# Performance work log

Measured on AMD Instinct MI355X. Metric: run time of the kernel, lower is better.

Reference implementation:

```python
import jax, jax.numpy as jnp
import numpy as np

N = 50000      # nodes
E = 800000     # edges (before self-loops)
H = 2          # attention heads
C = 64         # hidden_channels (per-head out since concat=False)
L = 3          # num_layers - 2 conv blocks
OUT = 128      # readout out_channels
G = 512        # num graphs
VOCAB = 100    # embedding table size
NEG_SLOPE = 0.2


def setup_inputs() -> dict:
    key = jax.random.key(0)
    ks = jax.random.split(key, 12)
    s = 1.0 / np.sqrt(C)
    x = jax.random.randint(ks[0], (N,), 0, VOCAB, dtype=jnp.int32)
    edge_index = jax.random.randint(ks[1], (2, E), 0, N, dtype=jnp.int32)
    batch = jnp.sort(jax.random.randint(ks[2], (N,), 0, G, dtype=jnp.int32))
    embed = jax.random.normal(ks[3], (VOCAB, C), dtype=jnp.float32) * s
    lin_W = jax.random.normal(ks[4], (L, C, C), dtype=jnp.float32) * s
    lin_b = jnp.zeros((L, C), dtype=jnp.float32)
    gat_Wl = jax.random.normal(ks[5], (L, C, H * C), dtype=jnp.float32) * s
    gat_bl = jnp.zeros((L, H * C), dtype=jnp.float32)
    gat_Wr = jax.random.normal(ks[6], (L, C, H * C), dtype=jnp.float32) * s
    gat_br = jnp.zeros((L, H * C), dtype=jnp.float32)
    gat_att = jax.random.normal(ks[7], (L, H, C), dtype=jnp.float32) * s
    gat_bias = jnp.zeros((L, C), dtype=jnp.float32)
    readout_W = jax.random.normal(ks[8], (C, OUT), dtype=jnp.float32) * s
    readout_b = jnp.zeros((OUT,), dtype=jnp.float32)
    return {"x": x, "edge_index": edge_index, "batch": batch, "num_graphs": G,
            "embed": embed, "lin_W": lin_W, "lin_b": lin_b,
            "gat_Wl": gat_Wl, "gat_bl": gat_bl, "gat_Wr": gat_Wr, "gat_br": gat_br,
            "gat_att": gat_att, "gat_bias": gat_bias,
            "readout_W": readout_W, "readout_b": readout_b}


def _gatv2_layer(h, src, dst, Wl, bl, Wr, br, att, bias):
    # lin_l -> source/message features, lin_r -> target features (PyG GATv2Conv)
    xl = (h @ Wl + bl).reshape(N, H, C)
    xr = (h @ Wr + br).reshape(N, H, C)
    # per-edge GATv2 score: a^T LeakyReLU(x_l[j] + x_r[i])
    e = jax.nn.leaky_relu(xl[src] + xr[dst], NEG_SLOPE)      # [E2,H,C]
    score = jnp.einsum('ehc,hc->eh', e, att)                 # [E2,H]
    # segment softmax over incoming edges of each dst node (stable)
    m = jax.lax.stop_gradient(jax.ops.segment_max(score, dst, num_segments=N))
    p = jnp.exp(score - m[dst])
    denom = jax.ops.segment_sum(p, dst, num_segments=N)      # [N,H]
    alpha = p / denom[dst]                                   # [E2,H]
    msg = xl[src] * alpha[:, :, None]                        # [E2,H,C]
    agg = jax.ops.segment_sum(msg, dst, num_segments=N)      # [N,H,C]
    return agg.mean(axis=1) + bias                           # concat=False -> head mean


def reference(x, edge_index, batch, num_graphs, embed, lin_W, lin_b,
              gat_Wl, gat_bl, gat_Wr, gat_br, gat_att, gat_bias,
              readout_W, readout_b):
    # add self loops (GATv2Conv default add_self_loops=True)
    loops = jnp.arange(N, dtype=edge_index.dtype)
    src = jnp.concatenate([edge_index[0], loops])
    dst = jnp.concatenate([edge_index[1], loops])
    h = embed[x]                                             # [N,C]
    for l in range(L):
        h = jax.nn.relu(h @ lin_W[l] + lin_b[l])             # dropout is a no-op in eval
        h = _gatv2_layer(h, src, dst, gat_Wl[l], gat_bl[l], gat_Wr[l], gat_br[l],
                         gat_att[l], gat_bias[l])
    out = h @ readout_W + readout_b                          # [N,OUT]
    return jax.ops.segment_sum(out, batch, num_segments=num_graphs)  # [G,OUT]
```

## Files before the change

### kernel.cpp

```cpp
#include <hip/hip_runtime.h>
#include <hip/hip_fp16.h>

#define N_NODES  50000
#define E_EDGES  800000
#define E_TOT    850000
#define H_HEADS  2
#define C_DIM    64
#define HC       128
#define L_LAYERS 3
#define OUT_DIM  128
#define G_GRAPHS 512
#define NEG_SLOPE 0.2f
#define NB       196
#define EPB      4096

typedef float v2f __attribute__((ext_vector_type(2)));

__device__ __forceinline__ void lds_fence() { asm volatile("" ::: "memory"); }

__global__ void init_kernel(float* __restrict__ out, int* __restrict__ bucket_counts) {
    int i = blockIdx.x * 256 + threadIdx.x;
    if (i < G_GRAPHS * OUT_DIM) out[i] = 0.f;
    if (blockIdx.x == 0) bucket_counts[threadIdx.x] = 0;
}

__global__ void bucket_count_kernel(const int* __restrict__ dsts, int* __restrict__ bucket_counts) {
    __shared__ int hist[256];
    int tid = threadIdx.x;
    hist[tid] = 0;
    __syncthreads();
    int ebase = blockIdx.x * EPB;
#pragma unroll
    for (int i = 0; i < 16; i++) {
        int e = ebase + i * 256 + tid;
        if (e < E_TOT) {
            int d = (e < E_EDGES) ? dsts[e] : e - E_EDGES;
            atomicAdd(&hist[d >> 8], 1);
        }
    }
    __syncthreads();
    if (hist[tid]) atomicAdd(&bucket_counts[tid], hist[tid]);
}

__global__ void scan196_kernel(const int* __restrict__ bucket_counts,
                               int* __restrict__ bwptr, int* __restrict__ bbase) {
    __shared__ int wsum[4];
    int tid = threadIdx.x;
    int lane = tid & 63, wid = tid >> 6;
    int cnt = (tid < NB) ? bucket_counts[tid] : 0;
    int v = cnt;
#pragma unroll
    for (int off = 1; off < 64; off <<= 1) {
        int t = __shfl_up(v, off, 64);
        if (lane >= off) v += t;
    }
    if (lane == 63) wsum[wid] = v;
    __syncthreads();
    int woff = 0;
#pragma unroll
    for (int w = 0; w < 4; w++) if (w < wid) woff += wsum[w];
    v += woff;
    if (tid < NB) { bwptr[tid] = v - cnt; bbase[tid] = v - cnt; }
    if (tid == 0) bbase[NB] = E_TOT;
}

__global__ void edge_partition_kernel(const int* __restrict__ srcs, const int* __restrict__ dsts,
                                      int* __restrict__ bwptr, unsigned int* __restrict__ ebuf) {
    __shared__ int hist[256];
    __shared__ int lscan[256];
    __shared__ int sExcl[256];
    __shared__ int lcnt[256];
    __shared__ int gbase[256];
    __shared__ unsigned int sval[EPB];
    __shared__ unsigned char sgid[EPB];
    int tid = threadIdx.x;
    int ebase = blockIdx.x * EPB;
    hist[tid] = 0;
    __syncthreads();
    unsigned int val[16];
    int gid[16];
#pragma unroll
    for (int i = 0; i < 16; i++) {
        int e = ebase + i * 256 + tid;
        if (e < E_TOT) {
            int s, d;
            if (e < E_EDGES) { s = srcs[e]; d = dsts[e]; }
            else             { s = d = e - E_EDGES; }
            val[i] = ((unsigned)s << 8) | (unsigned)(d & 255);
            gid[i] = d >> 8;
            atomicAdd(&hist[gid[i]], 1);
        } else gid[i] = -1;
    }
    __syncthreads();
    lscan[tid] = hist[tid];
    __syncthreads();
#pragma unroll
    for (int off = 1; off < 256; off <<= 1) {
        int t = (tid >= off) ? lscan[tid - off] : 0;
        __syncthreads();
        lscan[tid] += t;
        __syncthreads();
    }
    sExcl[tid] = lscan[tid] - hist[tid];
    lcnt[tid] = 0;
    __syncthreads();
#pragma unroll
    for (int i = 0; i < 16; i++) {
        if (gid[i] >= 0) {
            int off = atomicAdd(&lcnt[gid[i]], 1);
            int idx = sExcl[gid[i]] + off;
            sval[idx] = val[i];
            sgid[idx] = (unsigned char)gid[i];
        }
    }
    if (tid < NB) {
        int c = hist[tid];
        gbase[tid] = c ? atomicAdd(&bwptr[tid], c) : 0;
    }
    __syncthreads();
    int total = lscan[255];
    for (int idx = tid; idx < total; idx += 256) {
        int g = sgid[idx];
        ebuf[gbase[g] + (idx - sExcl[g])] = sval[idx];
    }
}

__global__ void bucket_csr_kernel(const unsigned int* __restrict__ ebuf,
                                  const int* __restrict__ bbase,
                                  int* __restrict__ row_ptr,
                                  unsigned short* __restrict__ src_sorted) {
    __shared__ int hist[256];
    __shared__ int lcnt[256];
    __shared__ int wsum[4];
    int g = blockIdx.x, tid = threadIdx.x;
    int n0 = g << 8;
    int nodes = min(256, N_NODES - n0);
    int b0 = bbase[g], b1 = bbase[g + 1];
    int cnt = b1 - b0;
    hist[tid] = 0;
    lcnt[tid] = 0;
    __syncthreads();
    for (int i = tid; i < cnt; i += 256) atomicAdd(&hist[ebuf[b0 + i] & 255], 1);
    __syncthreads();
    int c = hist[tid];
    int v = c;
    int lane = tid & 63, wid = tid >> 6;
#pragma unroll
    for (int off = 1; off < 64; off <<= 1) {
        int t = __shfl_up(v, off, 64);
        if (lane >= off) v += t;
    }
    if (lane == 63) wsum[wid] = v;
    __syncthreads();
    int woff = 0;
#pragma unroll
    for (int w = 0; w < 4; w++) if (w < wid) woff += wsum[w];
    v += woff;
    int nbase = b0 + v - c;
    if (tid < nodes) row_ptr[n0 + tid] = nbase;
    if (g == NB - 1 && tid == 0) row_ptr[N_NODES] = E_TOT;
    __syncthreads();
    hist[tid] = nbase;
    __syncthreads();
    for (int i = tid; i < cnt; i += 256) {
        unsigned int e = ebuf[b0 + i];
        int dl = e & 255;
        int slot = hist[dl] + atomicAdd(&lcnt[dl], 1);
        src_sorted[slot] = (unsigned short)(e >> 8);
    }
}

__global__ void layer_lin_kernel(const float* __restrict__ h,
                                 const int* __restrict__ xs, const float* __restrict__ etab,
                                 int use_embed,
                                 const float* __restrict__ W, const float* __restrict__ b,
                                 const float* __restrict__ Wl, const float* __restrict__ bl,
                                 const float* __restrict__ Wr, const float* __restrict__ br,
                                 __half* __restrict__ xlh, float* __restrict__ xri) {
    __shared__ float sH[16 * 64];
    __shared__ float sH2[16 * 64];
    int tid = threadIdx.x;
    int base = blockIdx.x * 16;
#pragma unroll
    for (int i = 0; i < 4; i++) {
        int idx = tid + i * 256;
        int nn = base + (idx >> 6);
        int cc = idx & 63;
        float hv = 0.f;
        if (nn < N_NODES)
            hv = use_embed ? etab[xs[nn] * 64 + cc] : h[(size_t)nn * 64 + cc];
        sH[idx] = hv;
    }
    __syncthreads();
    {
        int c = tid & 63, g = tid >> 6;
        float a0 = b[c], a1 = a0, a2 = a0, a3 = a0;
        for (int k = 0; k < 64; k++) {
            float wv = W[k * 64 + c];
            a0 = fmaf(sH[(g * 4 + 0) * 64 + k], wv, a0);
            a1 = fmaf(sH[(g * 4 + 1) * 64 + k], wv, a1);
            a2 = fmaf(sH[(g * 4 + 2) * 64 + k], wv, a2);
            a3 = fmaf(sH[(g * 4 + 3) * 64 + k], wv, a3);
        }
        sH2[(g * 4 + 0) * 64 + c] = fmaxf(a0, 0.f);
        sH2[(g * 4 + 1) * 64 + c] = fmaxf(a1, 0.f);
        sH2[(g * 4 + 2) * 64 + c] = fmaxf(a2, 0.f);
        sH2[(g * 4 + 3) * 64 + c] = fmaxf(a3, 0.f);
    }
    __syncthreads();
    {
        int j = tid & 127, gg = tid >> 7;
        float accl[8], accr[8];
#pragma unroll
        for (int n = 0; n < 8; n++) { accl[n] = bl[j]; accr[n] = br[j]; }
        for (int k = 0; k < 64; k++) {
            float wl = Wl[k * 128 + j], wr = Wr[k * 128 + j];
#pragma unroll
            for (int n = 0; n < 8; n++) {
                float hv = sH2[(gg * 8 + n) * 64 + k];
                accl[n] = fmaf(hv, wl, accl[n]);
                accr[n] = fmaf(hv, wr, accr[n]);
            }
        }
        int hh = j >> 6, c = j & 63;
#pragma unroll
        for (int n = 0; n < 8; n++) {
            int node = base + gg * 8 + n;
            if (node < N_NODES) {
                size_t o = (size_t)node * 128 + c * 2 + hh;
                xlh[o] = __float2half(accl[n]);
                xri[o] = accr[n];
            }
        }
    }
}

__global__ void gat_kernel(const __half2* __restrict__ xlh, const float2* __restrict__ xr2,
                           const float* __restrict__ att, const int* __restrict__ row_ptr,
                           const unsigned short* __restrict__ src_sorted,
                           const float* __restrict__ bias,
                           float* __restrict__ h_out) {
    __shared__ __align__(16) float cbuf[4][8 * 132];
    int w = threadIdx.x >> 6;
    int d = blockIdx.x * 4 + w;
    if (d >= N_NODES) return;
    int lane = threadIdx.x & 63;
    int r0 = row_ptr[d], r1 = row_ptr[d + 1];
    float2 vrf = xr2[(size_t)d * 64 + lane];
    v2f vr2 = {vrf.x, vrf.y};
    v2f att2 = {att[lane], att[64 + lane]};
    float* cb = cbuf[w];
    int e_of = lane >> 3, p = lane & 7;

    float dpx = 0.f, dpy = 0.f;
    v2f ac0 = {0.f, 0.f}, ac1 = {0.f, 0.f};

#define GAT_LOAD(V, CB) do {                                                    \
        int lim_ = nchunk - 1;                                                  \
        _Pragma("unroll")                                                       \
        for (int e = 0; e < 8; e++) {                                           \
            int ee_ = (CB) + e;                                                 \
            int sv_ = __builtin_amdgcn_readlane(idx, (ee_ < nchunk) ? ee_ : lim_); \
            V[e] = xlh[(size_t)sv_ * 64 + lane];                                \
        }                                                                       \
    } while (0)

#define GAT_PROC(V, CB) do {                                                    \
        int rem_ = nchunk - (CB);                                               \
        v2f vf8[8];                                                             \
        _Pragma("unroll")                                                       \
        for (int e = 0; e < 8; e++) {                                           \
            float2 vf_ = __half22float2(V[e]);                                  \
            v2f vl2 = {vf_.x, vf_.y};                                           \
            vf8[e] = vl2;                                                       \
            v2f z = vl2 + vr2;                                                  \
            v2f t = __builtin_elementwise_max(z, z * NEG_SLOPE) * att2;         \
            *(v2f*)&cb[e * 132 + 2 * lane] = t;                                 \
        }                                                                       \
        lds_fence();                                                            \
        v2f s2 = {0.f, 0.f};                                                    \
        {                                                                       \
            const float4* row_ = (const float4*)&cb[e_of * 132 + p * 16];       \
            _Pragma("unroll")                                                   \
            for (int j = 0; j < 4; j++) {                                       \
                float4 f = row_[j];                                             \
                s2 += (v2f){f.x, f.y};                                          \
                s2 += (v2f){f.z, f.w};                                          \
            }                                                                   \
        }                                                                       \
        lds_fence();                                                            \
        _Pragma("unroll")                                                       \
        for (int off = 1; off <= 4; off <<= 1) {                                \
            v2f o_;                                                             \
            o_.x = __shfl_xor(s2.x, off, 64);                                   \
            o_.y = __shfl_xor(s2.y, off, 64);                                   \
            s2 += o_;                                                           \
        }                                                                       \
        float sx = s2.x, sy = s2.y;                                             \
        if (e_of >= rem_) { sx = -INFINITY; sy = -INFINITY; }                   \
        float wx = __expf(sx), wy = __expf(sy);                                 \
        dpx += wx; dpy += wy;                                                   \
        _Pragma("unroll")                                                       \
        for (int e = 0; e < 8; e++) {                                           \
            float swx = __int_as_float(__builtin_amdgcn_readlane(__float_as_int(wx), 8 * e)); \
            float swy = __int_as_float(__builtin_amdgcn_readlane(__float_as_int(wy), 8 * e)); \
            v2f w2 = {swx, swy};                                                \
            if (e & 1) ac1 = __builtin_elementwise_fma(w2, vf8[e], ac1);        \
            else       ac0 = __builtin_elementwise_fma(w2, vf8[e], ac0);        \
        }                                                                       \
    } while (0)

    for (int base = r0; base < r1; base += 64) {
        int a = base + lane;
        int idx = (int)src_sorted[(a < r1) ? a : (r1 - 1)];
        int nchunk = min(64, r1 - base);
        __half2 va[8], vb[8];
        GAT_LOAD(va, 0);
        int cb_i = 0;
        for (;;) {
            int nx = cb_i + 8;
            if (nx < nchunk) {
                GAT_LOAD(vb, nx);
                GAT_PROC(va, cb_i);
                cb_i = nx;
            } else {
                GAT_PROC(va, cb_i);
                break;
            }
            nx = cb_i + 8;
            if (nx < nchunk) {
                GAT_LOAD(va, nx);
                GAT_PROC(vb, cb_i);
                cb_i = nx;
            } else {
                GAT_PROC(vb, cb_i);
                break;
            }
        }
    }
#undef GAT_LOAD
#undef GAT_PROC

#pragma unroll
    for (int off = 8; off <= 32; off <<= 1) {
        dpx += __shfl_xor(dpx, off, 64);
        dpy += __shfl_xor(dpy, off, 64);
    }
    v2f acc = ac0 + ac1;
    h_out[(size_t)d * 64 + lane] = (acc.x / dpx + acc.y / dpy) * 0.5f + bias[lane];
}

__global__ void readout_kernel(const float* __restrict__ h, const float* __restrict__ W,
                               const float* __restrict__ b, const int* __restrict__ batch,
                               float* __restrict__ out) {
    __shared__ float sH[16 * 64];
    __shared__ int sB[16];
    int tid = threadIdx.x;
    int base = blockIdx.x * 16;
#pragma unroll
    for (int i = 0; i < 4; i++) {
        int idx = tid + i * 256;
        int nn = base + (idx >> 6);
        sH[idx] = (nn < N_NODES) ? h[(size_t)nn * 64 + (idx & 63)] : 0.f;
    }
    if (tid < 16) sB[tid] = (base + tid < N_NODES) ? batch[base + tid] : -1;
    __syncthreads();
    int j = tid & 127, gg = tid >> 7;
    float acc[8];
#pragma unroll
    for (int n = 0; n < 8; n++) acc[n] = b[j];
    for (int k = 0; k < 64; k++) {
        float wv = W[k * OUT_DIM + j];
#pragma unroll
        for (int n = 0; n < 8; n++) acc[n] = fmaf(sH[(gg * 8 + n) * 64 + k], wv, acc[n]);
    }
    float run = 0.f; int curb = -2;
#pragma unroll
    for (int n = 0; n < 8; n++) {
        int node = base + gg * 8 + n;
        int bb = (node < N_NODES) ? sB[gg * 8 + n] : -1;
        if (bb != curb) {
            if (curb >= 0) atomicAdd(&out[curb * OUT_DIM + j], run);
            run = 0.f; curb = bb;
        }
        if (bb >= 0) run += acc[n];
    }
    if (curb >= 0) atomicAdd(&out[curb * OUT_DIM + j], run);
}

extern "C" void kernel_launch(void* const* d_in, const int* in_sizes, int n_in,
                              void* d_out, int out_size, void* d_ws, size_t ws_size,
                              hipStream_t stream) {
    const int*   x        = (const int*)d_in[0];
    const int*   edge     = (const int*)d_in[1];
    const int*   batch    = (const int*)d_in[2];
    const float* embed    = (const float*)d_in[4];
    const float* lin_W    = (const float*)d_in[5];
    const float* lin_b    = (const float*)d_in[6];
    const float* gat_Wl   = (const float*)d_in[7];
    const float* gat_bl   = (const float*)d_in[8];
    const float* gat_Wr   = (const float*)d_in[9];
    const float* gat_br   = (const float*)d_in[10];
    const float* gat_att  = (const float*)d_in[11];
    const float* gat_bias = (const float*)d_in[12];
    const float* ro_W     = (const float*)d_in[13];
    const float* ro_b     = (const float*)d_in[14];
    float* out = (float*)d_out;

    const int* srcs = edge;
    const int* dsts = edge + E_EDGES;

    float* h    = (float*)d_ws;
    __half* xlh = (__half*)(h + (size_t)N_NODES * 64);
    float* xr   = (float*)((char*)xlh + (size_t)N_NODES * HC * sizeof(__half));
    int* row_ptr       = (int*)(xr + (size_t)N_NODES * HC);
    int* bwptr         = row_ptr + N_NODES + 1;
    int* bbase         = bwptr + 256;
    int* bucket_counts = bbase + 256;
    unsigned int* ebuf = (unsigned int*)(bucket_counts + 256);
    unsigned short* src_sorted = (unsigned short*)(ebuf + E_TOT);

    const int T = 256;
    const int gInit = (G_GRAPHS * OUT_DIM + 255) / 256;
    const int gPart = (E_TOT + EPB - 1) / EPB;
    const int gLin  = (N_NODES + 15) / 16;
    const int gGat  = (N_NODES + 3) / 4;

    init_kernel<<<gInit, T, 0, stream>>>(out, bucket_counts);
    bucket_count_kernel<<<gPart, T, 0, stream>>>(dsts, bucket_counts);
    scan196_kernel<<<1, T, 0, stream>>>(bucket_counts, bwptr, bbase);
    edge_partition_kernel<<<gPart, T, 0, stream>>>(srcs, dsts, bwptr, ebuf);
    bucket_csr_kernel<<<NB, T, 0, stream>>>(ebuf, bbase, row_ptr, src_sorted);

    for (int l = 0; l < L_LAYERS; l++) {
        layer_lin_kernel<<<gLin, T, 0, stream>>>(
            h, x, embed, (l == 0) ? 1 : 0,
            lin_W + (size_t)l * 64 * 64, lin_b + (size_t)l * 64,
            gat_Wl + (size_t)l * 64 * 128, gat_bl + (size_t)l * 128,
            gat_Wr + (size_t)l * 64 * 128, gat_br + (size_t)l * 128,
            xlh, xr);
        gat_kernel<<<gGat, T, 0, stream>>>(
            (const __half2*)xlh, (const float2*)xr, gat_att + (size_t)l * HC,
            row_ptr, src_sorted, gat_bias + (size_t)l * 64, h);
    }

    readout_kernel<<<gLin, T, 0, stream>>>(h, ro_W, ro_b, batch, out);
}
```

Measured before the change: 407.8 us.

## Store xr in fp16, pack lin FMAs into v2f, shrink gat blocks to 128 threads

The target projection xr is now stored as fp16 instead of fp32, which halves its write traffic in the linear kernel and its read traffic in the GAT kernel. The linear kernel's FMAs are packed into two-wide float vectors so the compiler can emit packed FMA instructions. The GAT kernel now launches 2-wave blocks of 128 threads instead of 4 waves, with launch bounds, to give finer scheduling granularity. Storing xr in fp16 adds rounding error to the attention scores.

After: 417.2 us. +2.3%, slower.

```diff
diff --git a/kernel.cpp b/kernel.cpp
--- a/kernel.cpp
+++ b/kernel.cpp
@@ -176,7 +176,7 @@
                                  const float* __restrict__ W, const float* __restrict__ b,
                                  const float* __restrict__ Wl, const float* __restrict__ bl,
                                  const float* __restrict__ Wr, const float* __restrict__ br,
-                                 __half* __restrict__ xlh, float* __restrict__ xri) {
+                                 __half* __restrict__ xlh, __half* __restrict__ xrh) {
     __shared__ float sH[16 * 64];
     __shared__ float sH2[16 * 64];
     int tid = threadIdx.x;
@@ -194,32 +194,32 @@
     __syncthreads();
     {
         int c = tid & 63, g = tid >> 6;
-        float a0 = b[c], a1 = a0, a2 = a0, a3 = a0;
+        v2f a01 = {b[c], b[c]}, a23 = a01;
         for (int k = 0; k < 64; k++) {
             float wv = W[k * 64 + c];
-            a0 = fmaf(sH[(g * 4 + 0) * 64 + k], wv, a0);
-            a1 = fmaf(sH[(g * 4 + 1) * 64 + k], wv, a1);
-            a2 = fmaf(sH[(g * 4 + 2) * 64 + k], wv, a2);
-            a3 = fmaf(sH[(g * 4 + 3) * 64 + k], wv, a3);
-        }
-        sH2[(g * 4 + 0) * 64 + c] = fmaxf(a0, 0.f);
-        sH2[(g * 4 + 1) * 64 + c] = fmaxf(a1, 0.f);
-        sH2[(g * 4 + 2) * 64 + c] = fmaxf(a2, 0.f);
-        sH2[(g * 4 + 3) * 64 + c] = fmaxf(a3, 0.f);
+            v2f w2 = {wv, wv};
+            a01 = __builtin_elementwise_fma(
+                (v2f){sH[(g * 4 + 0) * 64 + k], sH[(g * 4 + 1) * 64 + k]}, w2, a01);
+            a23 = __builtin_elementwise_fma(
+                (v2f){sH[(g * 4 + 2) * 64 + k], sH[(g * 4 + 3) * 64 + k]}, w2, a23);
+        }
+        sH2[(g * 4 + 0) * 64 + c] = fmaxf(a01.x, 0.f);
+        sH2[(g * 4 + 1) * 64 + c] = fmaxf(a01.y, 0.f);
+        sH2[(g * 4 + 2) * 64 + c] = fmaxf(a23.x, 0.f);
+        sH2[(g * 4 + 3) * 64 + c] = fmaxf(a23.y, 0.f);
     }
     __syncthreads();
     {
         int j = tid & 127, gg = tid >> 7;
-        float accl[8], accr[8];
-#pragma unroll
-        for (int n = 0; n < 8; n++) { accl[n] = bl[j]; accr[n] = br[j]; }
+        v2f acc_lr[8];
+#pragma unroll
+        for (int n = 0; n < 8; n++) acc_lr[n] = (v2f){bl[j], br[j]};
         for (int k = 0; k < 64; k++) {
-            float wl = Wl[k * 128 + j], wr = Wr[k * 128 + j];
+            v2f w2 = {Wl[k * 128 + j], Wr[k * 128 + j]};
 #pragma unroll
             for (int n = 0; n < 8; n++) {
                 float hv = sH2[(gg * 8 + n) * 64 + k];
-                accl[n] = fmaf(hv, wl, accl[n]);
-                accr[n] = fmaf(hv, wr, accr[n]);
+                acc_lr[n] = __builtin_elementwise_fma((v2f){hv, hv}, w2, acc_lr[n]);
             }
         }
         int hh = j >> 6, c = j & 63;
@@ -228,25 +228,26 @@
             int node = base + gg * 8 + n;
             if (node < N_NODES) {
                 size_t o = (size_t)node * 128 + c * 2 + hh;
-                xlh[o] = __float2half(accl[n]);
-                xri[o] = accr[n];
+                xlh[o] = __float2half(acc_lr[n].x);
+                xrh[o] = __float2half(acc_lr[n].y);
             }
         }
     }
 }
 
-__global__ void gat_kernel(const __half2* __restrict__ xlh, const float2* __restrict__ xr2,
-                           const float* __restrict__ att, const int* __restrict__ row_ptr,
-                           const unsigned short* __restrict__ src_sorted,
-                           const float* __restrict__ bias,
-                           float* __restrict__ h_out) {
-    __shared__ __align__(16) float cbuf[4][8 * 132];
+__global__ void __launch_bounds__(128)
+gat_kernel(const __half2* __restrict__ xlh, const __half2* __restrict__ xrh2,
+           const float* __restrict__ att, const int* __restrict__ row_ptr,
+           const unsigned short* __restrict__ src_sorted,
+           const float* __restrict__ bias,
+           float* __restrict__ h_out) {
+    __shared__ __align__(16) float cbuf[2][8 * 132];
     int w = threadIdx.x >> 6;
-    int d = blockIdx.x * 4 + w;
+    int d = blockIdx.x * 2 + w;
     if (d >= N_NODES) return;
     int lane = threadIdx.x & 63;
     int r0 = row_ptr[d], r1 = row_ptr[d + 1];
-    float2 vrf = xr2[(size_t)d * 64 + lane];
+    float2 vrf = __half22float2(xrh2[(size_t)d * 64 + lane]);
     v2f vr2 = {vrf.x, vrf.y};
     v2f att2 = {att[lane], att[64 + lane]};
     float* cb = cbuf[w];
@@ -412,8 +413,8 @@
 
     float* h    = (float*)d_ws;
     __half* xlh = (__half*)(h + (size_t)N_NODES * 64);
-    float* xr   = (float*)((char*)xlh + (size_t)N_NODES * HC * sizeof(__half));
-    int* row_ptr       = (int*)(xr + (size_t)N_NODES * HC);
+    __half* xrh = xlh + (size_t)N_NODES * HC;
+    int* row_ptr       = (int*)(xrh + (size_t)N_NODES * HC);
     int* bwptr         = row_ptr + N_NODES + 1;
     int* bbase         = bwptr + 256;
     int* bucket_counts = bbase + 256;
@@ -424,7 +425,7 @@
     const int gInit = (G_GRAPHS * OUT_DIM + 255) / 256;
     const int gPart = (E_TOT + EPB - 1) / EPB;
     const int gLin  = (N_NODES + 15) / 16;
-    const int gGat  = (N_NODES + 3) / 4;
+    const int gGat  = (N_NODES + 1) / 2;
 
     init_kernel<<<gInit, T, 0, stream>>>(out, bucket_counts);
     bucket_count_kernel<<<gPart, T, 0, stream>>>(dsts, bucket_counts);
@@ -438,9 +439,9 @@
             lin_W + (size_t)l * 64 * 64, lin_b + (size_t)l * 64,
             gat_Wl + (size_t)l * 64 * 128, gat_bl + (size_t)l * 128,
             gat_Wr + (size_t)l * 64 * 128, gat_br + (size_t)l * 128,
-            xlh, xr);
-        gat_kernel<<<gGat, T, 0, stream>>>(
-            (const __half2*)xlh, (const float2*)xr, gat_att + (size_t)l * HC,
+            xlh, xrh);
+        gat_kernel<<<gGat, 128, 0, stream>>>(
+            (const __half2*)xlh, (const __half2*)xrh, gat_att + (size_t)l * HC,
             row_ptr, src_sorted, gat_bias + (size_t)l * 64, h);
     }
 
```
